# Optimization experiments

Measured on AMD Instinct MI355X. Metric: run time of the kernel, lower is better.

Reference implementation:

```python
import jax, jax.numpy as jnp
import numpy as np

GROUPS = 2
NUM_CODEWORDS = 320
TAU = 2.0  # curr_temp = max_temp at init
EPS = 1e-7


def setup_inputs() -> dict:
    key = jax.random.key(0)
    k1, k2, k3, k4 = jax.random.split(key, 4)
    B, T, D = 16, 2048, 768
    GK = GROUPS * NUM_CODEWORDS  # 640
    VAR_DIM = 128  # vq_dim // groups
    return {
        "x": jax.random.normal(k1, (B, T, D), dtype=jnp.float32),
        "W": jax.random.normal(k2, (D, GK), dtype=jnp.float32),  # nn.init.normal_(weight, std=1)
        "b": jnp.zeros((GK,), dtype=jnp.float32),
        "codebook": jax.random.uniform(k3, (1, GK, VAR_DIM), dtype=jnp.float32),  # self.vars, uniform init
        "uniform_noise": jax.random.uniform(k4, (B * T, GROUPS, NUM_CODEWORDS), dtype=jnp.float32),
    }


def reference(x, W, b, codebook, uniform_noise):
    B, T, D = x.shape
    BT = B * T
    # weight projection: [BT, D] @ [D, G*K] -> logits viewed as [BT, G, K]
    logits = (x.reshape(BT, D) @ W + b).reshape(BT, GROUPS, NUM_CODEWORDS)

    # hard code perplexity (no-grad in original)
    hard_x = jax.lax.stop_gradient(
        jax.nn.one_hot(jnp.argmax(logits, axis=-1), NUM_CODEWORDS, dtype=logits.dtype)
    )  # [BT, G, K]
    hard_probs = hard_x.mean(axis=0)  # [G, K]
    code_perplexity = jnp.exp(-jnp.sum(hard_probs * jnp.log(hard_probs + EPS), axis=-1)).sum()

    # soft (prob) perplexity
    avg_probs = jax.nn.softmax(logits, axis=-1).mean(axis=0)  # [G, K]
    prob_perplexity = jnp.exp(-jnp.sum(avg_probs * jnp.log(avg_probs + EPS), axis=-1)).sum()

    # gumbel-softmax (training path, hard=True, straight-through)
    u = uniform_noise * (1.0 - 2e-6) + 1e-6  # keep in (0,1)
    g = -jnp.log(-jnp.log(u))
    y_soft = jax.nn.softmax((logits + g) / TAU, axis=-1)  # [BT, G, K]
    y_hard = jax.nn.one_hot(jnp.argmax(y_soft, axis=-1), NUM_CODEWORDS, dtype=y_soft.dtype)
    y = y_hard + y_soft - jax.lax.stop_gradient(y_soft)

    # codebook combine: equivalent to (y.unsqueeze(-1) * vars).view(BT,G,K,d).sum(-2)
    cb = codebook.reshape(GROUPS, NUM_CODEWORDS, -1)  # combine_groups=False
    out = jnp.einsum('ngk,gkd->ngd', y, cb).reshape(B, T, -1)  # [B, T, vq_dim]
    return out, code_perplexity, prob_perplexity
```

## Files before the change

### kernel.cpp

```cpp
#include <hip/hip_runtime.h>
#include <cmath>

#define D_K 768
#define GK 640
#define KC_N 24
#define NC_N 40

typedef _Float16 f16x8 __attribute__((ext_vector_type(8)));
typedef float f32x4 __attribute__((ext_vector_type(4)));

__global__ __launch_bounds__(256) void prep_kernel(const float* __restrict__ W,
        unsigned* __restrict__ bins, _Float16* __restrict__ WH, _Float16* __restrict__ WL) {
    int t = blockIdx.x * 256 + threadIdx.x;
    if (t < 1280) bins[t] = 0u;
    int fid = t >> 6;
    int l = t & 63;
    int kc = fid / NC_N, nc = fid - kc * NC_N;
    int n = nc * 16 + (l & 15);
    int k0 = kc * 32 + (l >> 4) * 8;
    f16x8 hi, lo;
#pragma unroll
    for (int j = 0; j < 8; ++j) {
        float wv = W[(size_t)(k0 + j) * GK + n];
        _Float16 h = (_Float16)wv;
        hi[j] = h;
        lo[j] = (_Float16)(wv - (float)h);
    }
    *(f16x8*)(WH + (size_t)fid * 512 + l * 8) = hi;
    *(f16x8*)(WL + (size_t)fid * 512 + l * 8) = lo;
}

__global__ __launch_bounds__(512) void main_kernel(
        const float* __restrict__ x, const float* __restrict__ bias,
        const float* __restrict__ noise, const float* __restrict__ cb,
        const _Float16* __restrict__ WH, const _Float16* __restrict__ WL,
        float* __restrict__ out, unsigned* __restrict__ counts, float* __restrict__ probsum)
{
    int tid = threadIdx.x;
    int w = tid >> 6;
    int l = tid & 63;
    int lrow = l >> 4;
    int lcol = l & 15;
    int r0 = blockIdx.x * 64;
    int ncb = w * 5;
    int g = w >> 2;

    f32x4 acc[4][5];
#pragma unroll
    for (int mc = 0; mc < 4; ++mc)
#pragma unroll
        for (int j = 0; j < 5; ++j) acc[mc][j] = (f32x4){0.f, 0.f, 0.f, 0.f};

    const float* xb = x + (size_t)(r0 + lcol) * D_K + lrow * 8;

    for (int kc = 0; kc < KC_N; ++kc) {
        f16x8 ah[4], al[4];
#pragma unroll
        for (int mc = 0; mc < 4; ++mc) {
            const float* p = xb + mc * (16 * D_K) + kc * 32;
            f32x4 v0 = *(const f32x4*)p;
            f32x4 v1 = *(const f32x4*)(p + 4);
#pragma unroll
            for (int j = 0; j < 4; ++j) {
                float f0 = v0[j];
                _Float16 h0 = (_Float16)f0;
                ah[mc][j] = h0; al[mc][j] = (_Float16)(f0 - (float)h0);
                float f1 = v1[j];
                _Float16 h1 = (_Float16)f1;
                ah[mc][4 + j] = h1; al[mc][4 + j] = (_Float16)(f1 - (float)h1);
            }
        }
        const _Float16* bh_p = WH + ((size_t)(kc * NC_N + ncb) * 64 + l) * 8;
        const _Float16* bl_p = WL + ((size_t)(kc * NC_N + ncb) * 64 + l) * 8;
#pragma unroll
        for (int j = 0; j < 5; ++j) {
            f16x8 bh = *(const f16x8*)(bh_p + j * 512);
            f16x8 bl = *(const f16x8*)(bl_p + j * 512);
#pragma unroll
            for (int mc = 0; mc < 4; ++mc) {
                acc[mc][j] = __builtin_amdgcn_mfma_f32_16x16x32_f16(ah[mc], bh, acc[mc][j], 0, 0, 0);
                acc[mc][j] = __builtin_amdgcn_mfma_f32_16x16x32_f16(al[mc], bh, acc[mc][j], 0, 0, 0);
                acc[mc][j] = __builtin_amdgcn_mfma_f32_16x16x32_f16(ah[mc], bl, acc[mc][j], 0, 0, 0);
            }
        }
    }

#pragma unroll
    for (int j = 0; j < 5; ++j) {
        float bb = bias[(ncb + j) * 16 + lcol];
#pragma unroll
        for (int mc = 0; mc < 4; ++mc)
#pragma unroll
            for (int r = 0; r < 4; ++r) acc[mc][j][r] += bb;
    }

    __shared__ float s_pmax[8][64];
    __shared__ int   s_pcol[8][64];
    __shared__ float s_pgmax[8][64];
    __shared__ int   s_pgcol[8][64];
    __shared__ float s_psum[8][64];
    __shared__ float s_fmax[128];
    __shared__ float s_fsum[128];
    __shared__ int   s_fgcol[128];
    __shared__ float s_bins[640];

#pragma unroll
    for (int mc = 0; mc < 4; ++mc) {
#pragma unroll
        for (int r = 0; r < 4; ++r) {
            int row = mc * 16 + lrow * 4 + r;
            float vmax = -3.4e38f; int vcol = 0;
            float gmax = -3.4e38f; int gcol = 0;
            const float* np = noise + (size_t)(r0 + row) * GK + ncb * 16 + lcol;
#pragma unroll
            for (int j = 0; j < 5; ++j) {
                float v = acc[mc][j][r];
                int c = (ncb + j) * 16 + lcol;
                if (v > vmax) { vmax = v; vcol = c; }
                float u = np[j * 16] * (1.0f - 2e-6f) + 1e-6f;
                float gn = -__logf(-__logf(u));
                float z = v + gn;
                if (z > gmax) { gmax = z; gcol = c; }
            }
#pragma unroll
            for (int off = 1; off < 16; off <<= 1) {
                float ov = __shfl_xor(vmax, off); int oc = __shfl_xor(vcol, off);
                if (ov > vmax || (ov == vmax && oc < vcol)) { vmax = ov; vcol = oc; }
                float og = __shfl_xor(gmax, off); int ogc = __shfl_xor(gcol, off);
                if (og > gmax || (og == gmax && ogc < gcol)) { gmax = og; gcol = ogc; }
            }
            if (lcol == 0) {
                s_pmax[w][row] = vmax; s_pcol[w][row] = vcol;
                s_pgmax[w][row] = gmax; s_pgcol[w][row] = gcol;
            }
        }
    }
    s_bins[tid] = 0.0f;
    if (tid < 128) s_bins[512 + tid] = 0.0f;
    __syncthreads();

    if (tid < 128) {
        int gg = tid >> 6, row = tid & 63;
        float vmax = -3.4e38f; int vcol = 0;
        float gmax = -3.4e38f; int gcol = 0;
        for (int ww = gg * 4; ww < gg * 4 + 4; ++ww) {
            float v = s_pmax[ww][row];
            if (v > vmax) { vmax = v; vcol = s_pcol[ww][row]; }
            float z = s_pgmax[ww][row];
            if (z > gmax) { gmax = z; gcol = s_pgcol[ww][row]; }
        }
        s_fmax[tid] = vmax;
        s_fgcol[tid] = gcol;
        atomicAdd(&counts[vcol], 1u);
    }
    __syncthreads();

#pragma unroll
    for (int mc = 0; mc < 4; ++mc) {
#pragma unroll
        for (int r = 0; r < 4; ++r) {
            int row = mc * 16 + lrow * 4 + r;
            float M = s_fmax[g * 64 + row];
            float s = 0.f;
#pragma unroll
            for (int j = 0; j < 5; ++j) s += __expf(acc[mc][j][r] - M);
#pragma unroll
            for (int off = 1; off < 16; off <<= 1) s += __shfl_xor(s, off);
            if (lcol == 0) s_psum[w][row] = s;
        }
    }
    __syncthreads();
    if (tid < 128) {
        int gg = tid >> 6, row = tid & 63;
        float S = 0.f;
        for (int ww = gg * 4; ww < gg * 4 + 4; ++ww) S += s_psum[ww][row];
        s_fsum[tid] = S;
    }
    __syncthreads();

#pragma unroll
    for (int mc = 0; mc < 4; ++mc) {
#pragma unroll
        for (int r = 0; r < 4; ++r) {
            int row = mc * 16 + lrow * 4 + r;
            float M = s_fmax[g * 64 + row];
            float invS = 1.0f / s_fsum[g * 64 + row];
#pragma unroll
            for (int j = 0; j < 5; ++j)
                atomicAdd(&s_bins[(ncb + j) * 16 + lcol], __expf(acc[mc][j][r] - M) * invS);
        }
    }
    __syncthreads();
    atomicAdd(&probsum[tid], s_bins[tid]);
    if (tid < 128) atomicAdd(&probsum[512 + tid], s_bins[512 + tid]);

    {
        int team = tid >> 2, jj = tid & 3;
        int row = team >> 1, gg = team & 1;
        int wcol = s_fgcol[gg * 64 + row];
        const f32x4* src = (const f32x4*)(cb + (size_t)wcol * 128);
        f32x4* dst = (f32x4*)(out + (size_t)(r0 + row) * 256 + gg * 128);
#pragma unroll
        for (int i = 0; i < 8; ++i) dst[i * 4 + jj] = src[i * 4 + jj];
    }
}

__global__ __launch_bounds__(640) void fin_kernel(const unsigned* __restrict__ counts,
        const float* __restrict__ probsum, float* __restrict__ out2) {
    __shared__ float sh[640], sp[640];
    int t = threadIdx.x;
    float ph = (float)counts[t] * (1.0f / 32768.0f);
    sh[t] = ph * logf(ph + 1e-7f);
    float pp = probsum[t] * (1.0f / 32768.0f);
    sp[t] = pp * logf(pp + 1e-7f);
    __syncthreads();
    if (t < 2) {
        const float* s = (t == 0) ? sh : sp;
        float e0 = 0.f, e1 = 0.f;
        for (int k = 0; k < 320; ++k) { e0 += s[k]; e1 += s[320 + k]; }
        out2[t] = expf(-e0) + expf(-e1);
    }
}

extern "C" void kernel_launch(void* const* d_in, const int* in_sizes, int n_in,
                              void* d_out, int out_size, void* d_ws, size_t ws_size,
                              hipStream_t stream) {
    const float* x     = (const float*)d_in[0];
    const float* W     = (const float*)d_in[1];
    const float* b     = (const float*)d_in[2];
    const float* cb    = (const float*)d_in[3];
    const float* noise = (const float*)d_in[4];
    float* out = (float*)d_out;

    char* ws = (char*)d_ws;
    unsigned* counts = (unsigned*)ws;
    float* probsum   = (float*)(ws + 2560);
    _Float16* WH     = (_Float16*)(ws + 8192);
    _Float16* WL     = (_Float16*)(ws + 8192 + 983040);

    hipLaunchKernelGGL(prep_kernel, dim3(240), dim3(256), 0, stream, W, counts, WH, WL);
    hipLaunchKernelGGL(main_kernel, dim3(512), dim3(512), 0, stream,
                       x, b, noise, cb, WH, WL, out, counts, probsum);
    hipLaunchKernelGGL(fin_kernel, dim3(1), dim3(640), 0, stream, counts, probsum, out + 8388608);
}
```

Measured before the change: 491.1 us.

## Split main kernel rows across 16 waves and software-prefetch x and W fragments

Doubles the block to 1024 threads so each wave handles 32 rows instead of 64, halving accumulator registers per wave and raising waves per CU. It adds register double-buffering, prefetching the next k-chunk of x and the next W fragment while the current MFMAs run, to hide global load latency. The reductions are reindexed for 16 waves, and the finalize kernel now sums entropy terms with a wave shuffle reduction instead of a serial loop. In exchange, every wave converts its own x rows while reading the same W fragments as one other wave, so W traffic per block doubles, and the larger block adds synchronisation cost.

```diff
diff --git a/kernel.cpp b/kernel.cpp
--- a/kernel.cpp
+++ b/kernel.cpp
@@ -30,7 +30,7 @@
     *(f16x8*)(WL + (size_t)fid * 512 + l * 8) = lo;
 }
 
-__global__ __launch_bounds__(512) void main_kernel(
+__global__ __launch_bounds__(1024, 4) void main_kernel(
         const float* __restrict__ x, const float* __restrict__ bias,
         const float* __restrict__ noise, const float* __restrict__ cb,
         const _Float16* __restrict__ WH, const _Float16* __restrict__ WL,
@@ -42,79 +42,89 @@
     int lrow = l >> 4;
     int lcol = l & 15;
     int r0 = blockIdx.x * 64;
-    int ncb = w * 5;
-    int g = w >> 2;
-
-    f32x4 acc[4][5];
-#pragma unroll
-    for (int mc = 0; mc < 4; ++mc)
-#pragma unroll
-        for (int j = 0; j < 5; ++j) acc[mc][j] = (f32x4){0.f, 0.f, 0.f, 0.f};
-
-    const float* xb = x + (size_t)(r0 + lcol) * D_K + lrow * 8;
+    int mch = w >> 3;
+    int wn = w & 7;
+    int ncb = wn * 5;
+    int g = wn >> 2;
+
+    f32x4 acc[2][5];
+#pragma unroll
+    for (int i = 0; i < 2; ++i)
+#pragma unroll
+        for (int j = 0; j < 5; ++j) acc[i][j] = (f32x4){0.f, 0.f, 0.f, 0.f};
+
+    const float* xb0 = x + (size_t)(r0 + mch * 32 + lcol) * D_K + lrow * 8;
+    const float* xb1 = xb0 + 16 * D_K;
+
+    f32x4 a00 = *(const f32x4*)xb0, a01 = *(const f32x4*)(xb0 + 4);
+    f32x4 a10 = *(const f32x4*)xb1, a11 = *(const f32x4*)(xb1 + 4);
 
     for (int kc = 0; kc < KC_N; ++kc) {
-        f16x8 ah[4], al[4];
-#pragma unroll
-        for (int mc = 0; mc < 4; ++mc) {
-            const float* p = xb + mc * (16 * D_K) + kc * 32;
-            f32x4 v0 = *(const f32x4*)p;
-            f32x4 v1 = *(const f32x4*)(p + 4);
-#pragma unroll
-            for (int j = 0; j < 4; ++j) {
-                float f0 = v0[j];
-                _Float16 h0 = (_Float16)f0;
-                ah[mc][j] = h0; al[mc][j] = (_Float16)(f0 - (float)h0);
-                float f1 = v1[j];
-                _Float16 h1 = (_Float16)f1;
-                ah[mc][4 + j] = h1; al[mc][4 + j] = (_Float16)(f1 - (float)h1);
-            }
-        }
+        int kn = (kc < KC_N - 1) ? kc + 1 : 0;
+        f32x4 n00 = *(const f32x4*)(xb0 + kn * 32), n01 = *(const f32x4*)(xb0 + kn * 32 + 4);
+        f32x4 n10 = *(const f32x4*)(xb1 + kn * 32), n11 = *(const f32x4*)(xb1 + kn * 32 + 4);
+
+        f16x8 ah[2], al[2];
+#pragma unroll
+        for (int j = 0; j < 4; ++j) {
+            float f;
+            _Float16 h;
+            f = a00[j]; h = (_Float16)f; ah[0][j] = h;     al[0][j] = (_Float16)(f - (float)h);
+            f = a01[j]; h = (_Float16)f; ah[0][4 + j] = h; al[0][4 + j] = (_Float16)(f - (float)h);
+            f = a10[j]; h = (_Float16)f; ah[1][j] = h;     al[1][j] = (_Float16)(f - (float)h);
+            f = a11[j]; h = (_Float16)f; ah[1][4 + j] = h; al[1][4 + j] = (_Float16)(f - (float)h);
+        }
+
         const _Float16* bh_p = WH + ((size_t)(kc * NC_N + ncb) * 64 + l) * 8;
         const _Float16* bl_p = WL + ((size_t)(kc * NC_N + ncb) * 64 + l) * 8;
+        f16x8 bh = *(const f16x8*)bh_p;
+        f16x8 bl = *(const f16x8*)bl_p;
 #pragma unroll
         for (int j = 0; j < 5; ++j) {
-            f16x8 bh = *(const f16x8*)(bh_p + j * 512);
-            f16x8 bl = *(const f16x8*)(bl_p + j * 512);
-#pragma unroll
-            for (int mc = 0; mc < 4; ++mc) {
-                acc[mc][j] = __builtin_amdgcn_mfma_f32_16x16x32_f16(ah[mc], bh, acc[mc][j], 0, 0, 0);
-                acc[mc][j] = __builtin_amdgcn_mfma_f32_16x16x32_f16(al[mc], bh, acc[mc][j], 0, 0, 0);
-                acc[mc][j] = __builtin_amdgcn_mfma_f32_16x16x32_f16(ah[mc], bl, acc[mc][j], 0, 0, 0);
-            }
-        }
+            int jn = (j < 4) ? j + 1 : 0;
+            f16x8 nbh = *(const f16x8*)(bh_p + jn * 512);
+            f16x8 nbl = *(const f16x8*)(bl_p + jn * 512);
+            acc[0][j] = __builtin_amdgcn_mfma_f32_16x16x32_f16(ah[0], bh, acc[0][j], 0, 0, 0);
+            acc[0][j] = __builtin_amdgcn_mfma_f32_16x16x32_f16(al[0], bh, acc[0][j], 0, 0, 0);
+            acc[0][j] = __builtin_amdgcn_mfma_f32_16x16x32_f16(ah[0], bl, acc[0][j], 0, 0, 0);
+            acc[1][j] = __builtin_amdgcn_mfma_f32_16x16x32_f16(ah[1], bh, acc[1][j], 0, 0, 0);
+            acc[1][j] = __builtin_amdgcn_mfma_f32_16x16x32_f16(al[1], bh, acc[1][j], 0, 0, 0);
+            acc[1][j] = __builtin_amdgcn_mfma_f32_16x16x32_f16(ah[1], bl, acc[1][j], 0, 0, 0);
+            bh = nbh; bl = nbl;
+        }
+        a00 = n00; a01 = n01; a10 = n10; a11 = n11;
     }
 
 #pragma unroll
     for (int j = 0; j < 5; ++j) {
         float bb = bias[(ncb + j) * 16 + lcol];
 #pragma unroll
-        for (int mc = 0; mc < 4; ++mc)
-#pragma unroll
-            for (int r = 0; r < 4; ++r) acc[mc][j][r] += bb;
-    }
-
-    __shared__ float s_pmax[8][64];
-    __shared__ int   s_pcol[8][64];
-    __shared__ float s_pgmax[8][64];
-    __shared__ int   s_pgcol[8][64];
-    __shared__ float s_psum[8][64];
+        for (int i = 0; i < 2; ++i)
+#pragma unroll
+            for (int r = 0; r < 4; ++r) acc[i][j][r] += bb;
+    }
+
+    __shared__ float s_pmax[16][64];
+    __shared__ int   s_pcol[16][64];
+    __shared__ float s_pgmax[16][64];
+    __shared__ int   s_pgcol[16][64];
+    __shared__ float s_psum[16][64];
     __shared__ float s_fmax[128];
     __shared__ float s_fsum[128];
     __shared__ int   s_fgcol[128];
     __shared__ float s_bins[640];
 
 #pragma unroll
-    for (int mc = 0; mc < 4; ++mc) {
+    for (int i = 0; i < 2; ++i) {
 #pragma unroll
         for (int r = 0; r < 4; ++r) {
-            int row = mc * 16 + lrow * 4 + r;
+            int row = mch * 32 + i * 16 + lrow * 4 + r;
             float vmax = -3.4e38f; int vcol = 0;
             float gmax = -3.4e38f; int gcol = 0;
             const float* np = noise + (size_t)(r0 + row) * GK + ncb * 16 + lcol;
 #pragma unroll
             for (int j = 0; j < 5; ++j) {
-                float v = acc[mc][j][r];
+                float v = acc[i][j][r];
                 int c = (ncb + j) * 16 + lcol;
                 if (v > vmax) { vmax = v; vcol = c; }
                 float u = np[j * 16] * (1.0f - 2e-6f) + 1e-6f;
@@ -135,15 +145,16 @@
             }
         }
     }
-    s_bins[tid] = 0.0f;
-    if (tid < 128) s_bins[512 + tid] = 0.0f;
+    if (tid < 640) s_bins[tid] = 0.0f;
     __syncthreads();
 
     if (tid < 128) {
         int gg = tid >> 6, row = tid & 63;
         float vmax = -3.4e38f; int vcol = 0;
         float gmax = -3.4e38f; int gcol = 0;
-        for (int ww = gg * 4; ww < gg * 4 + 4; ++ww) {
+        int wb = (row >> 5) * 8 + gg * 4;
+        for (int i = 0; i < 4; ++i) {
+            int ww = wb + i;
             float v = s_pmax[ww][row];
             if (v > vmax) { vmax = v; vcol = s_pcol[ww][row]; }
             float z = s_pgmax[ww][row];
@@ -156,14 +167,14 @@
     __syncthreads();
 
 #pragma unroll
-    for (int mc = 0; mc < 4; ++mc) {
+    for (int i = 0; i < 2; ++i) {
 #pragma unroll
         for (int r = 0; r < 4; ++r) {
-            int row = mc * 16 + lrow * 4 + r;
+            int row = mch * 32 + i * 16 + lrow * 4 + r;
             float M = s_fmax[g * 64 + row];
             float s = 0.f;
 #pragma unroll
-            for (int j = 0; j < 5; ++j) s += __expf(acc[mc][j][r] - M);
+            for (int j = 0; j < 5; ++j) s += __expf(acc[i][j][r] - M);
 #pragma unroll
             for (int off = 1; off < 16; off <<= 1) s += __shfl_xor(s, off);
             if (lcol == 0) s_psum[w][row] = s;
@@ -172,54 +183,62 @@
     __syncthreads();
     if (tid < 128) {
         int gg = tid >> 6, row = tid & 63;
+        int wb = (row >> 5) * 8 + gg * 4;
         float S = 0.f;
-        for (int ww = gg * 4; ww < gg * 4 + 4; ++ww) S += s_psum[ww][row];
+        for (int i = 0; i < 4; ++i) S += s_psum[wb + i][row];
         s_fsum[tid] = S;
     }
     __syncthreads();
 
 #pragma unroll
-    for (int mc = 0; mc < 4; ++mc) {
+    for (int i = 0; i < 2; ++i) {
 #pragma unroll
         for (int r = 0; r < 4; ++r) {
-            int row = mc * 16 + lrow * 4 + r;
+            int row = mch * 32 + i * 16 + lrow * 4 + r;
             float M = s_fmax[g * 64 + row];
             float invS = 1.0f / s_fsum[g * 64 + row];
 #pragma unroll
             for (int j = 0; j < 5; ++j)
-                atomicAdd(&s_bins[(ncb + j) * 16 + lcol], __expf(acc[mc][j][r] - M) * invS);
-        }
-    }
-    __syncthreads();
-    atomicAdd(&probsum[tid], s_bins[tid]);
-    if (tid < 128) atomicAdd(&probsum[512 + tid], s_bins[512 + tid]);
+                atomicAdd(&s_bins[(ncb + j) * 16 + lcol], __expf(acc[i][j][r] - M) * invS);
+        }
+    }
+    __syncthreads();
+    if (tid < 640) atomicAdd(&probsum[tid], s_bins[tid]);
 
     {
-        int team = tid >> 2, jj = tid & 3;
+        int team = tid >> 3, jj = tid & 7;
         int row = team >> 1, gg = team & 1;
         int wcol = s_fgcol[gg * 64 + row];
         const f32x4* src = (const f32x4*)(cb + (size_t)wcol * 128);
         f32x4* dst = (f32x4*)(out + (size_t)(r0 + row) * 256 + gg * 128);
 #pragma unroll
-        for (int i = 0; i < 8; ++i) dst[i * 4 + jj] = src[i * 4 + jj];
+        for (int k = 0; k < 4; ++k) dst[k * 8 + jj] = src[k * 8 + jj];
     }
 }
 
 __global__ __launch_bounds__(640) void fin_kernel(const unsigned* __restrict__ counts,
         const float* __restrict__ probsum, float* __restrict__ out2) {
-    __shared__ float sh[640], sp[640];
+    __shared__ float sh[640], sp[640], sred[4];
     int t = threadIdx.x;
     float ph = (float)counts[t] * (1.0f / 32768.0f);
     sh[t] = ph * logf(ph + 1e-7f);
     float pp = probsum[t] * (1.0f / 32768.0f);
     sp[t] = pp * logf(pp + 1e-7f);
     __syncthreads();
-    if (t < 2) {
-        const float* s = (t == 0) ? sh : sp;
-        float e0 = 0.f, e1 = 0.f;
-        for (int k = 0; k < 320; ++k) { e0 += s[k]; e1 += s[320 + k]; }
-        out2[t] = expf(-e0) + expf(-e1);
-    }
+    if (t < 256) {
+        int seg = t >> 6;
+        int l = t & 63;
+        const float* s = (seg & 2) ? sp : sh;
+        int base = (seg & 1) * 320;
+        float v = 0.f;
+#pragma unroll
+        for (int k = 0; k < 5; ++k) v += s[base + l + 64 * k];
+#pragma unroll
+        for (int off = 1; off < 64; off <<= 1) v += __shfl_xor(v, off);
+        if (l == 0) sred[seg] = v;
+    }
+    __syncthreads();
+    if (t < 2) out2[t] = expf(-sred[t * 2]) + expf(-sred[t * 2 + 1]);
 }
 
 extern "C" void kernel_launch(void* const* d_in, const int* in_sizes, int n_in,
@@ -239,7 +258,7 @@
     _Float16* WL     = (_Float16*)(ws + 8192 + 983040);
 
     hipLaunchKernelGGL(prep_kernel, dim3(240), dim3(256), 0, stream, W, counts, WH, WL);
-    hipLaunchKernelGGL(main_kernel, dim3(512), dim3(512), 0, stream,
+    hipLaunchKernelGGL(main_kernel, dim3(512), dim3(1024), 0, stream,
                        x, b, noise, cb, WH, WL, out, counts, probsum);
     hipLaunchKernelGGL(fin_kernel, dim3(1), dim3(640), 0, stream, counts, probsum, out + 8388608);
 }
```

New measurement: 490.5 us. No clear change (-0.1%).
